# Optimization experiments

Measured on AMD Instinct MI355X. Metric: run time of the kernel, lower is better.

## Reference

```python
import jax, jax.numpy as jnp
from jax import lax
import numpy as np

N_ITERS = 200        # FISTA iterations (replaces per-row CVXPY solves)
BISECT_ITERS = 50    # bisection steps for capped-simplex projection
POWER_ITERS = 30     # power iterations for Lipschitz estimate


def _project_capped_simplex(v, lower, upper):
    """Project v (shape [N]) onto {x : sum(x)=1, lower<=x<=upper} via bisection on the dual shift tau."""
    lo = jnp.min(v) - upper
    hi = jnp.max(v) - lower

    def body(carry, _):
        lo, hi = carry
        mid = 0.5 * (lo + hi)
        s = jnp.sum(jnp.clip(v - mid, lower, upper))  # decreasing in mid
        lo = jnp.where(s > 1.0, mid, lo)
        hi = jnp.where(s > 1.0, hi, mid)
        return (lo, hi), None

    (lo, hi), _ = lax.scan(body, (lo, hi), None, length=BISECT_ITERS)
    tau = 0.5 * (lo + hi)
    return jnp.clip(v - tau, lower, upper)


def _solve_qp_batched(A, Y, lower, upper):
    """Batched solve of min_x ||x @ A - y||^2 s.t. sum(x)=1, lower<=x<=upper,
    one QP per row y of Y. A: [N,D], Y: [N,D] -> X: [N,N]. FISTA with exact
    capped-simplex projection; faithful to the per-row CVXPY QP in the source."""
    N = A.shape[0]
    Q = A @ A.T            # [N,N] Hessian/2
    C = Y @ A.T            # [N,N] linear term

    # Lipschitz constant of gradient = 2 * lambda_max(Q), via power iteration.
    v = jnp.ones((N,), A.dtype) / N

    def pw(v, _):
        w = Q @ v
        return w / (jnp.linalg.norm(w) + 1e-12), None

    v, _ = lax.scan(pw, v, None, length=POWER_ITERS)
    lmax = v @ (Q @ v)
    step = 1.0 / (2.0 * lmax + 1e-12)

    proj = jax.vmap(lambda r: _project_capped_simplex(r, lower, upper))
    X0 = jnp.full((N, N), 1.0 / N, A.dtype)  # feasible start (uniform simplex point)

    def fista(carry, _):
        X, Z, t = carry
        G = 2.0 * (Z @ Q - C)                 # grad of ||z A - y||^2 wrt z, all rows at once
        Xn = proj(Z - step * G)
        tn = 0.5 * (1.0 + jnp.sqrt(1.0 + 4.0 * t * t))
        Zn = Xn + ((t - 1.0) / tn) * (Xn - X)
        return (Xn, Zn, tn), None

    (X, _, _), _ = lax.scan(fista, (X0, X0, jnp.asarray(1.0, A.dtype)), None, length=N_ITERS)
    return X


def setup_inputs() -> dict:
    key = jax.random.key(0)
    k1, k2 = jax.random.split(key)
    N, D = 2048, 512
    fea1 = jax.random.normal(k1, (N, D), jnp.float32)
    fea2 = jax.random.normal(k2, (N, D), jnp.float32)
    return {"fea1": fea1, "fea2": fea2}


def reference(fea1, fea2):
    lower, upper = 0.0, 1.0
    nfea1 = fea1 / jnp.linalg.norm(fea1, axis=1, keepdims=True)
    nfea2 = fea2 / jnp.linalg.norm(fea2, axis=1, keepdims=True)
    # Solver operates on detached features in the original (numpy/CVXPY).
    XX = _solve_qp_batched(lax.stop_gradient(nfea2), lax.stop_gradient(nfea1), lower, upper)
    XX = lax.stop_gradient(XX)  # mirrors XX.detach() in the source
    distance = -jnp.mean((XX @ nfea2 - nfea1) ** 2)  # -MSELoss
    return distance
```

## Files before the change

kernel.cpp:

```cpp
#include <hip/hip_runtime.h>
#include <cmath>

#define N 2048
#define D 512
#define N_ITERS 200
#define NEWTON_ITERS 16
#define POWER_ITERS 30

typedef unsigned short u16;
typedef __bf16 bf16x8 __attribute__((ext_vector_type(8)));
typedef float f32x4 __attribute__((ext_vector_type(4)));

__device__ __forceinline__ float wave_reduce_sum(float x) {
#pragma unroll
  for (int o = 32; o > 0; o >>= 1) x += __shfl_xor(x, o, 64);
  return x;
}

__device__ __forceinline__ u16 f2b(float f) {
  unsigned int u = __float_as_uint(f);
  u = (u + 0x7FFFu + ((u >> 16) & 1u)) >> 16;
  return (u16)u;
}

__device__ __forceinline__ float b2f(unsigned int lo16) {
  return __uint_as_float((lo16 & 0xffffu) << 16);
}

__device__ __forceinline__ void gload16(const u16* g, u16* l) {
  __builtin_amdgcn_global_load_lds(
      (const __attribute__((address_space(1))) unsigned int*)g,
      (__attribute__((address_space(3))) unsigned int*)l, 16, 0, 0);
}

__global__ __launch_bounds__(256) void rownorm_kernel(const float* __restrict__ fea1,
                                                      const float* __restrict__ fea2,
                                                      float* __restrict__ Y,
                                                      float* __restrict__ A) {
  int b = blockIdx.x;
  int row = b & (N - 1);
  const float* src = (b < N) ? fea1 : fea2;
  float* dst = (b < N) ? Y : A;
  const float2* s2 = (const float2*)(src + (size_t)row * D);
  float2* d2 = (float2*)(dst + (size_t)row * D);
  int t = threadIdx.x;
  float2 v = s2[t];
  float ss = v.x * v.x + v.y * v.y;
  ss = wave_reduce_sum(ss);
  __shared__ float sred[4];
  int wid = t >> 6, lane = t & 63;
  if (lane == 0) sred[wid] = ss;
  __syncthreads();
  if (t == 0) sred[0] = sred[0] + sred[1] + sred[2] + sred[3];
  __syncthreads();
  float inv = 1.0f / sqrtf(sred[0]);
  d2[t] = make_float2(v.x * inv, v.y * inv);
}

__global__ __launch_bounds__(256) void prep_kernel(const float* __restrict__ A,
                                                   u16* __restrict__ Ab,
                                                   u16* __restrict__ AbT) {
  __shared__ float tile[32][33];
  int c0 = blockIdx.x * 32, r0 = blockIdx.y * 32;
  int tid = threadIdx.x;
  int r = tid >> 3, q = tid & 7;
  float4 v = *(const float4*)&A[(size_t)(r0 + r) * D + c0 + q * 4];
  tile[r][q * 4 + 0] = v.x; tile[r][q * 4 + 1] = v.y;
  tile[r][q * 4 + 2] = v.z; tile[r][q * 4 + 3] = v.w;
  ushort4 b4 = make_ushort4(f2b(v.x), f2b(v.y), f2b(v.z), f2b(v.w));
  *(ushort4*)&Ab[(size_t)(r0 + r) * D + c0 + q * 4] = b4;
  __syncthreads();
  int c = tid >> 3, qq = tid & 7;
  ushort4 t4 = make_ushort4(f2b(tile[qq * 4 + 0][c]), f2b(tile[qq * 4 + 1][c]),
                            f2b(tile[qq * 4 + 2][c]), f2b(tile[qq * 4 + 3][c]));
  *(ushort4*)&AbT[(size_t)(c0 + c) * N + r0 + qq * 4] = t4;
}

__global__ __launch_bounds__(256) void fill_init(u16* __restrict__ Zb, u16* __restrict__ Xb,
                                                 float* __restrict__ v) {
  const float c = 1.0f / (float)N;
  const unsigned int cw = (unsigned int)f2b(c);
  const unsigned int pp = cw | (cw << 16);
  size_t i = (size_t)blockIdx.x * blockDim.x + threadIdx.x;
  uint4 val = make_uint4(pp, pp, pp, pp);
  ((uint4*)Zb)[i] = val;
  ((uint4*)Xb)[i] = val;
  if (i < N) v[i] = c;
}

__global__ __launch_bounds__(256) void atv_kernel(const u16* __restrict__ Ab,
                                                  const float* __restrict__ v,
                                                  float* __restrict__ u) {
  __shared__ float part[4][64];
  int lane = threadIdx.x & 63, wid = threadIdx.x >> 6;
  int d = blockIdx.x * 64 + lane;
  float acc = 0.f;
  int r0 = wid * 512;
  for (int i = 0; i < 512; ++i) {
    int r = r0 + i;
    acc = fmaf(b2f(Ab[(size_t)r * D + d]), v[r], acc);
  }
  part[wid][lane] = acc;
  __syncthreads();
  if (wid == 0) u[d] = part[0][lane] + part[1][lane] + part[2][lane] + part[3][lane];
}

__global__ __launch_bounds__(256) void av_kernel(const u16* __restrict__ Ab,
                                                 const float* __restrict__ u,
                                                 float* __restrict__ w) {
  int wid = threadIdx.x >> 6, lane = threadIdx.x & 63;
  int row = blockIdx.x * 4 + wid;
  uint4 q = *(const uint4*)&Ab[(size_t)row * D + lane * 8];
  float4 u0 = *(const float4*)&u[lane * 8];
  float4 u1 = *(const float4*)&u[lane * 8 + 4];
  float acc = 0.f;
  acc = fmaf(b2f(q.x), u0.x, acc);
  acc = fmaf(b2f(q.x >> 16), u0.y, acc);
  acc = fmaf(b2f(q.y), u0.z, acc);
  acc = fmaf(b2f(q.y >> 16), u0.w, acc);
  acc = fmaf(b2f(q.z), u1.x, acc);
  acc = fmaf(b2f(q.z >> 16), u1.y, acc);
  acc = fmaf(b2f(q.w), u1.z, acc);
  acc = fmaf(b2f(q.w >> 16), u1.w, acc);
  acc = wave_reduce_sum(acc);
  if (lane == 0) w[row] = acc * 0.0625f;
}

__global__ __launch_bounds__(1024) void rayleigh_kernel(const float* __restrict__ v,
                                                        const float* __restrict__ w,
                                                        float* __restrict__ step) {
  int t = threadIdx.x;
  float a0 = v[t], a1 = v[t + 1024];
  float b0 = w[t], b1 = w[t + 1024];
  float s1 = a0 * b0 + a1 * b1;
  float s2 = a0 * a0 + a1 * a1;
  s1 = wave_reduce_sum(s1);
  s2 = wave_reduce_sum(s2);
  __shared__ float r1[16], r2[16];
  int wid = t >> 6, lane = t & 63;
  if (lane == 0) { r1[wid] = s1; r2[wid] = s2; }
  __syncthreads();
  if (t == 0) {
    float t1 = 0.f, t2 = 0.f;
#pragma unroll
    for (int i = 0; i < 16; ++i) { t1 += r1[i]; t2 += r2[i]; }
    float lam = 16.0f * t1 / t2;
    step[0] = 1.0f / (2.0f * lam + 1e-12f);
  }
}


template <int FOUT>
__global__ __launch_bounds__(256) void gemm1_mfma(const u16* __restrict__ Am,
                                                  const u16* __restrict__ Bm,
                                                  const float* __restrict__ Y,
                                                  u16* __restrict__ outb,
                                                  float* __restrict__ outf) {
  __shared__ u16 lds[2 * 16384];
  const int tid = threadIdx.x, lane = tid & 63, wid = tid >> 6;
  const int row0 = blockIdx.y * 64, col0 = blockIdx.x * 64;
  const int wr = (wid >> 1) * 32, wc = (wid & 1) * 32;
  const int fr = lane & 15, h = lane >> 4;
  const int grow = lane >> 4, gslot = lane & 15;
  f32x4 acc[2][2] = {};

#define G1_STAGE(BUF, T)                                                        \
  {                                                                             \
    const int k0 = (T) * 128;                                                   \
    _Pragma("unroll") for (int q = 0; q < 4; ++q) {                             \
      const int m = wid * 4 + q;                                                \
      const int r = m * 4 + grow;                                               \
      const int kl = (gslot ^ (r & 15)) * 8;                                    \
      gload16(&Am[(size_t)(row0 + r) * 2048 + k0 + kl],                         \
              &lds[(BUF) * 16384 + m * 512]);                                   \
      gload16(&Bm[(size_t)(col0 + r) * 2048 + k0 + kl],                         \
              &lds[(BUF) * 16384 + 8192 + m * 512]);                            \
    }                                                                           \
  }

  G1_STAGE(0, 0);
  __syncthreads();
#pragma unroll 2
  for (int t = 0; t < 16; ++t) {
    const int buf = (t & 1) * 16384;
    if (t < 15) G1_STAGE((t & 1) ^ 1, t + 1);
    bf16x8 af[2][4], bg[2][4];
#pragma unroll
    for (int i = 0; i < 2; ++i) {
      const int r = wr + i * 16 + fr;
#pragma unroll
      for (int ks = 0; ks < 4; ++ks)
        af[i][ks] = *(const bf16x8*)&lds[buf + r * 128 + ((((ks << 2) + h) ^ (r & 15)) << 3)];
    }
#pragma unroll
    for (int j = 0; j < 2; ++j) {
      const int c = wc + j * 16 + fr;
#pragma unroll
      for (int ks = 0; ks < 4; ++ks)
        bg[j][ks] = *(const bf16x8*)&lds[buf + 8192 + c * 128 + ((((ks << 2) + h) ^ (c & 15)) << 3)];
    }
#pragma unroll
    for (int ks = 0; ks < 4; ++ks)
#pragma unroll
      for (int i = 0; i < 2; ++i)
#pragma unroll
        for (int j = 0; j < 2; ++j)
          acc[i][j] = __builtin_amdgcn_mfma_f32_16x16x32_bf16(af[i][ks], bg[j][ks], acc[i][j], 0, 0, 0);
    __syncthreads();
  }
#pragma unroll
  for (int i = 0; i < 2; ++i)
#pragma unroll
    for (int j = 0; j < 2; ++j)
#pragma unroll
      for (int g = 0; g < 4; ++g) {
        int r = row0 + wr + i * 16 + h * 4 + g;
        int c = col0 + wc + j * 16 + fr;
        float val = acc[i][j][g] - Y[(size_t)r * D + c];
        if (FOUT) outf[(size_t)r * D + c] = val;
        else      outb[(size_t)r * D + c] = f2b(val);
      }
#undef G1_STAGE
}

__global__ __launch_bounds__(512) void gemm2_mfma(const u16* __restrict__ Tb,
                                                  const u16* __restrict__ Ab,
                                                  u16* __restrict__ Gb) {
  __shared__ u16 lds[2 * 16384];
  const int tid = threadIdx.x, lane = tid & 63, wid = tid >> 6;
  const int row0 = blockIdx.y * 128, col0 = blockIdx.x * 128;
  const int wr = (wid >> 2) * 64, wc = (wid & 3) * 32;
  const int fr = lane & 15, h = lane >> 4;
  const int grow = lane >> 3, gslot = lane & 7;
  f32x4 acc[4][2] = {};

#define G2_STAGE(BUF, T)                                                        \
  {                                                                             \
    const int k0 = (T) * 64;                                                    \
    _Pragma("unroll") for (int q = 0; q < 2; ++q) {                             \
      const int m = wid * 2 + q;                                                \
      const int r = m * 8 + grow;                                               \
      const int kl = (gslot ^ (r & 7)) * 8;                                     \
      gload16(&Tb[(size_t)(row0 + r) * 512 + k0 + kl],                          \
              &lds[(BUF) * 16384 + m * 512]);                                   \
      gload16(&Ab[(size_t)(col0 + r) * 512 + k0 + kl],                          \
              &lds[(BUF) * 16384 + 8192 + m * 512]);                            \
    }                                                                           \
  }

  G2_STAGE(0, 0);
  __syncthreads();
#pragma unroll 2
  for (int t = 0; t < 8; ++t) {
    const int buf = (t & 1) * 16384;
    if (t < 7) G2_STAGE((t & 1) ^ 1, t + 1);
    bf16x8 af[4][2], bg[2][2];
#pragma unroll
    for (int i = 0; i < 4; ++i) {
      const int r = wr + i * 16 + fr;
#pragma unroll
      for (int ks = 0; ks < 2; ++ks)
        af[i][ks] = *(const bf16x8*)&lds[buf + r * 64 + ((((ks << 2) + h) ^ (r & 7)) << 3)];
    }
#pragma unroll
    for (int j = 0; j < 2; ++j) {
      const int c = wc + j * 16 + fr;
#pragma unroll
      for (int ks = 0; ks < 2; ++ks)
        bg[j][ks] = *(const bf16x8*)&lds[buf + 8192 + c * 64 + ((((ks << 2) + h) ^ (c & 7)) << 3)];
    }
#pragma unroll
    for (int ks = 0; ks < 2; ++ks)
#pragma unroll
      for (int i = 0; i < 4; ++i)
#pragma unroll
        for (int j = 0; j < 2; ++j)
          acc[i][j] = __builtin_amdgcn_mfma_f32_16x16x32_bf16(af[i][ks], bg[j][ks], acc[i][j], 0, 0, 0);
    __syncthreads();
  }
#pragma unroll
  for (int i = 0; i < 4; ++i)
#pragma unroll
    for (int j = 0; j < 2; ++j)
#pragma unroll
      for (int g = 0; g < 4; ++g) {
        int r = row0 + wr + i * 16 + h * 4 + g;
        int c = col0 + wc + j * 16 + fr;
        Gb[(size_t)r * N + c] = f2b(acc[i][j][g]);
      }
#undef G2_STAGE
}

__global__ __launch_bounds__(256) void prox_kernel(const u16* __restrict__ Gb,
                                                   u16* __restrict__ Zb,
                                                   u16* __restrict__ Xb,
                                                   const float* __restrict__ stepp,
                                                   float beta) {
  const int wid = threadIdx.x >> 6, lane = threadIdx.x & 63;
  const int row = blockIdx.x * 4 + wid;
  const size_t rb = (size_t)row * N;
  const float s2 = 2.0f * stepp[0];
  float v[32], xo[32];
  float mn = 1e30f, mx = -1e30f;
#pragma unroll
  for (int c = 0; c < 4; ++c) {
    const int base = c * 512 + lane * 8;
    uint4 zu = *(const uint4*)&Zb[rb + base];
    uint4 gu = *(const uint4*)&Gb[rb + base];
    uint4 xu = *(const uint4*)&Xb[rb + base];
    const unsigned int zw[4] = {zu.x, zu.y, zu.z, zu.w};
    const unsigned int gw[4] = {gu.x, gu.y, gu.z, gu.w};
    const unsigned int xw[4] = {xu.x, xu.y, xu.z, xu.w};
#pragma unroll
    for (int w = 0; w < 4; ++w) {
      int e = c * 8 + w * 2;
      float v0 = b2f(zw[w]) - s2 * b2f(gw[w]);
      float v1 = __uint_as_float(zw[w] & 0xffff0000u) - s2 * __uint_as_float(gw[w] & 0xffff0000u);
      v[e] = v0; v[e + 1] = v1;
      xo[e] = b2f(xw[w]); xo[e + 1] = __uint_as_float(xw[w] & 0xffff0000u);
      mn = fminf(mn, fminf(v0, v1));
      mx = fmaxf(mx, fmaxf(v0, v1));
    }
  }
#pragma unroll
  for (int o = 32; o > 0; o >>= 1) {
    mn = fminf(mn, __shfl_xor(mn, o, 64));
    mx = fmaxf(mx, __shfl_xor(mx, o, 64));
  }
  float lo = mn - 1.0f, hi = mx;
  float mid = 0.5f * (lo + hi);
#pragma unroll 1
  for (int it = 0; it < NEWTON_ITERS; ++it) {
    float s = 0.f, cnt = 0.f;
#pragma unroll
    for (int e = 0; e < 32; ++e) {
      float d = v[e] - mid;
      s += fminf(fmaxf(d, 0.f), 1.f);
      cnt += (d > 0.f && d < 1.f) ? 1.f : 0.f;
    }
    s = wave_reduce_sum(s);
    cnt = wave_reduce_sum(cnt);
    bool gt = s > 1.0f;
    lo = gt ? mid : lo;
    hi = gt ? hi : mid;
    float prop = mid + (s - 1.0f) / fmaxf(cnt, 0.5f);
    mid = (prop > lo && prop < hi) ? prop : 0.5f * (lo + hi);
  }
  float tau = mid;
#pragma unroll
  for (int c = 0; c < 4; ++c) {
    const int base = c * 512 + lane * 8;
    unsigned int xp[4], zp[4];
#pragma unroll
    for (int q = 0; q < 8; ++q) {
      int e = c * 8 + q;
      float x = fminf(fmaxf(v[e] - tau, 0.f), 1.f);
      float zn = x + beta * (x - xo[e]);
      unsigned int xb = (unsigned int)f2b(x);
      unsigned int zb = (unsigned int)f2b(zn);
      if (q & 1) { xp[q >> 1] |= xb << 16; zp[q >> 1] |= zb << 16; }
      else       { xp[q >> 1] = xb;        zp[q >> 1] = zb; }
    }
    *(uint4*)&Xb[rb + base] = make_uint4(xp[0], xp[1], xp[2], xp[3]);
    *(uint4*)&Zb[rb + base] = make_uint4(zp[0], zp[1], zp[2], zp[3]);
  }
}

__global__ void zero_out_kernel(float* __restrict__ out) {
  if (threadIdx.x == 0 && blockIdx.x == 0) out[0] = 0.f;
}

__global__ __launch_bounds__(256) void mse_reduce_kernel(const float* __restrict__ T,
                                                         float* __restrict__ out) {
  size_t i = (size_t)blockIdx.x * blockDim.x + threadIdx.x;
  size_t total = (size_t)N * D;
  size_t stride = (size_t)gridDim.x * blockDim.x;
  float acc = 0.f;
  for (size_t idx = i; idx < total; idx += stride) {
    float t = T[idx];
    acc = fmaf(t, t, acc);
  }
  acc = wave_reduce_sum(acc);
  __shared__ float sred[4];
  int wid = threadIdx.x >> 6, lane = threadIdx.x & 63;
  if (lane == 0) sred[wid] = acc;
  __syncthreads();
  if (threadIdx.x == 0) {
    float tot = sred[0] + sred[1] + sred[2] + sred[3];
    atomicAdd(out, -tot / (float)((size_t)N * D));
  }
}

extern "C" void kernel_launch(void* const* d_in, const int* in_sizes, int n_in,
                              void* d_out, int out_size, void* d_ws, size_t ws_size,
                              hipStream_t stream) {
  const float* fea1 = (const float*)d_in[0];
  const float* fea2 = (const float*)d_in[1];
  float* out = (float*)d_out;
  float* ws = (float*)d_ws;

  float* A   = ws;
  float* Y   = A + (size_t)N * D;
  float* T32 = Y + (size_t)N * D;
  float* vv  = T32 + (size_t)N * D;
  float* wv  = vv + N;
  float* uu  = wv + N;
  float* sp  = uu + D;
  u16* Zb    = (u16*)(sp + 16);
  u16* Gb    = Zb + (size_t)N * N;
  u16* Xb    = Gb + (size_t)N * N;
  u16* Tb    = Xb + (size_t)N * N;
  u16* Ab    = Tb + (size_t)N * D;
  u16* AbT   = Ab + (size_t)N * D;

  rownorm_kernel<<<2 * N, 256, 0, stream>>>(fea1, fea2, Y, A);
  prep_kernel<<<dim3(D / 32, N / 32), 256, 0, stream>>>(A, Ab, AbT);
  fill_init<<<(N * N / 8) / 256, 256, 0, stream>>>(Zb, Xb, vv);

  float* pv = vv;
  float* pw = wv;
  for (int it = 0; it < POWER_ITERS; ++it) {
    atv_kernel<<<D / 64, 256, 0, stream>>>(Ab, pv, uu);
    av_kernel<<<N / 4, 256, 0, stream>>>(Ab, uu, pw);
    float* tmp = pv; pv = pw; pw = tmp;
  }
  atv_kernel<<<D / 64, 256, 0, stream>>>(Ab, pv, uu);
  av_kernel<<<N / 4, 256, 0, stream>>>(Ab, uu, pw);
  rayleigh_kernel<<<1, 1024, 0, stream>>>(pv, pw, sp);

  float t = 1.0f;
  for (int it = 0; it < N_ITERS; ++it) {
    float tn = 0.5f * (1.0f + sqrtf(1.0f + 4.0f * t * t));
    float beta = (t - 1.0f) / tn;
    t = tn;
    gemm1_mfma<0><<<dim3(D / 64, N / 64), 256, 0, stream>>>(Zb, AbT, Y, Tb, T32);
    gemm2_mfma<<<dim3(N / 128, N / 128), 512, 0, stream>>>(Tb, Ab, Gb);
    prox_kernel<<<N / 4, 256, 0, stream>>>(Gb, Zb, Xb, sp, beta);
  }

  gemm1_mfma<1><<<dim3(D / 64, N / 64), 256, 0, stream>>>(Xb, AbT, Y, Tb, T32);
  zero_out_kernel<<<1, 64, 0, stream>>>(out);
  mse_reduce_kernel<<<512, 256, 0, stream>>>(T32, out);
}
```

Baseline: 10.44 ms.

## Fuse FISTA loop into one persistent kernel with grid barriers

```diff
diff --git a/kernel.cpp b/kernel.cpp
--- a/kernel.cpp
+++ b/kernel.cpp
@@ -6,6 +6,7 @@
 #define N_ITERS 200
 #define NEWTON_ITERS 16
 #define POWER_ITERS 30
+#define NBLOCKS 256
 
 typedef unsigned short u16;
 typedef __bf16 bf16x8 __attribute__((ext_vector_type(8)));
@@ -31,6 +32,23 @@
   __builtin_amdgcn_global_load_lds(
       (const __attribute__((address_space(1))) unsigned int*)g,
       (__attribute__((address_space(3))) unsigned int*)l, 16, 0, 0);
+}
+
+__device__ __forceinline__ void grid_barrier(unsigned int* bar) {
+  __syncthreads();
+  if (threadIdx.x == 0) {
+    unsigned int g = __hip_atomic_load(&bar[1], __ATOMIC_RELAXED, __HIP_MEMORY_SCOPE_AGENT);
+    unsigned int a = __hip_atomic_fetch_add(&bar[0], 1u, __ATOMIC_ACQ_REL, __HIP_MEMORY_SCOPE_AGENT);
+    if (a + 1u == (unsigned int)NBLOCKS) {
+      __hip_atomic_store(&bar[0], 0u, __ATOMIC_RELAXED, __HIP_MEMORY_SCOPE_AGENT);
+      __hip_atomic_store(&bar[1], g + 1u, __ATOMIC_RELEASE, __HIP_MEMORY_SCOPE_AGENT);
+    } else {
+      while (__hip_atomic_load(&bar[1], __ATOMIC_ACQUIRE, __HIP_MEMORY_SCOPE_AGENT) == g) {
+        __builtin_amdgcn_s_sleep(8);
+      }
+    }
+  }
+  __syncthreads();
 }
 
 __global__ __launch_bounds__(256) void rownorm_kernel(const float* __restrict__ fea1,
@@ -77,7 +95,8 @@
 }
 
 __global__ __launch_bounds__(256) void fill_init(u16* __restrict__ Zb, u16* __restrict__ Xb,
-                                                 float* __restrict__ v) {
+                                                 float* __restrict__ v,
+                                                 unsigned int* __restrict__ bar) {
   const float c = 1.0f / (float)N;
   const unsigned int cw = (unsigned int)f2b(c);
   const unsigned int pp = cw | (cw << 16);
@@ -86,6 +105,7 @@
   ((uint4*)Zb)[i] = val;
   ((uint4*)Xb)[i] = val;
   if (i < N) v[i] = c;
+  if (i < 4) bar[i] = 0u;
 }
 
 __global__ __launch_bounds__(256) void atv_kernel(const u16* __restrict__ Ab,
@@ -151,40 +171,37 @@
 
 
 template <int FOUT>
-__global__ __launch_bounds__(256) void gemm1_mfma(const u16* __restrict__ Am,
-                                                  const u16* __restrict__ Bm,
-                                                  const float* __restrict__ Y,
-                                                  u16* __restrict__ outb,
-                                                  float* __restrict__ outf) {
-  __shared__ u16 lds[2 * 16384];
-  const int tid = threadIdx.x, lane = tid & 63, wid = tid >> 6;
-  const int row0 = blockIdx.y * 64, col0 = blockIdx.x * 64;
-  const int wr = (wid >> 1) * 32, wc = (wid & 1) * 32;
+__device__ __forceinline__ void phase_g1(u16* lds, const u16* __restrict__ Am,
+                                         const u16* __restrict__ Bm,
+                                         const float* __restrict__ Y,
+                                         u16* __restrict__ outb, float* __restrict__ outf,
+                                         int bid, int tid) {
+  const int lane = tid & 63, wid = tid >> 6;
+  const int row0 = (bid >> 3) * 64, col0 = (bid & 7) * 64;
+  const int wr = (wid >> 2) * 32, wc = (wid & 3) * 16;
   const int fr = lane & 15, h = lane >> 4;
   const int grow = lane >> 4, gslot = lane & 15;
-  f32x4 acc[2][2] = {};
-
-#define G1_STAGE(BUF, T)                                                        \
-  {                                                                             \
-    const int k0 = (T) * 128;                                                   \
-    _Pragma("unroll") for (int q = 0; q < 4; ++q) {                             \
-      const int m = wid * 4 + q;                                                \
-      const int r = m * 4 + grow;                                               \
-      const int kl = (gslot ^ (r & 15)) * 8;                                    \
-      gload16(&Am[(size_t)(row0 + r) * 2048 + k0 + kl],                         \
-              &lds[(BUF) * 16384 + m * 512]);                                   \
-      gload16(&Bm[(size_t)(col0 + r) * 2048 + k0 + kl],                         \
-              &lds[(BUF) * 16384 + 8192 + m * 512]);                            \
-    }                                                                           \
-  }
-
-  G1_STAGE(0, 0);
+  f32x4 acc[2] = {};
+
+#define G1S(BUF, T)                                                              \
+  {                                                                              \
+    const int k0 = (T) * 128;                                                    \
+    _Pragma("unroll") for (int q = 0; q < 2; ++q) {                              \
+      const int m = wid * 2 + q;                                                 \
+      const int r = m * 4 + grow;                                                \
+      const int kl = (gslot ^ (r & 15)) * 8;                                     \
+      gload16(&Am[(size_t)(row0 + r) * 2048 + k0 + kl], &lds[(BUF)*16384 + m*512]);        \
+      gload16(&Bm[(size_t)(col0 + r) * 2048 + k0 + kl], &lds[(BUF)*16384 + 8192 + m*512]); \
+    }                                                                            \
+  }
+
+  G1S(0, 0);
   __syncthreads();
 #pragma unroll 2
   for (int t = 0; t < 16; ++t) {
     const int buf = (t & 1) * 16384;
-    if (t < 15) G1_STAGE((t & 1) ^ 1, t + 1);
-    bf16x8 af[2][4], bg[2][4];
+    if (t < 15) G1S((t & 1) ^ 1, t + 1);
+    bf16x8 af[2][4], bg[4];
 #pragma unroll
     for (int i = 0; i < 2; ++i) {
       const int r = wr + i * 16 + fr;
@@ -192,68 +209,60 @@
       for (int ks = 0; ks < 4; ++ks)
         af[i][ks] = *(const bf16x8*)&lds[buf + r * 128 + ((((ks << 2) + h) ^ (r & 15)) << 3)];
     }
-#pragma unroll
-    for (int j = 0; j < 2; ++j) {
-      const int c = wc + j * 16 + fr;
+    {
+      const int c = wc + fr;
 #pragma unroll
       for (int ks = 0; ks < 4; ++ks)
-        bg[j][ks] = *(const bf16x8*)&lds[buf + 8192 + c * 128 + ((((ks << 2) + h) ^ (c & 15)) << 3)];
+        bg[ks] = *(const bf16x8*)&lds[buf + 8192 + c * 128 + ((((ks << 2) + h) ^ (c & 15)) << 3)];
     }
 #pragma unroll
     for (int ks = 0; ks < 4; ++ks)
 #pragma unroll
       for (int i = 0; i < 2; ++i)
-#pragma unroll
-        for (int j = 0; j < 2; ++j)
-          acc[i][j] = __builtin_amdgcn_mfma_f32_16x16x32_bf16(af[i][ks], bg[j][ks], acc[i][j], 0, 0, 0);
+        acc[i] = __builtin_amdgcn_mfma_f32_16x16x32_bf16(af[i][ks], bg[ks], acc[i], 0, 0, 0);
     __syncthreads();
   }
 #pragma unroll
   for (int i = 0; i < 2; ++i)
 #pragma unroll
-    for (int j = 0; j < 2; ++j)
-#pragma unroll
-      for (int g = 0; g < 4; ++g) {
-        int r = row0 + wr + i * 16 + h * 4 + g;
-        int c = col0 + wc + j * 16 + fr;
-        float val = acc[i][j][g] - Y[(size_t)r * D + c];
-        if (FOUT) outf[(size_t)r * D + c] = val;
-        else      outb[(size_t)r * D + c] = f2b(val);
-      }
-#undef G1_STAGE
-}
-
-__global__ __launch_bounds__(512) void gemm2_mfma(const u16* __restrict__ Tb,
-                                                  const u16* __restrict__ Ab,
-                                                  u16* __restrict__ Gb) {
-  __shared__ u16 lds[2 * 16384];
-  const int tid = threadIdx.x, lane = tid & 63, wid = tid >> 6;
-  const int row0 = blockIdx.y * 128, col0 = blockIdx.x * 128;
+    for (int g = 0; g < 4; ++g) {
+      int r = row0 + wr + i * 16 + h * 4 + g;
+      int c = col0 + wc + fr;
+      float val = acc[i][g] - Y[(size_t)r * D + c];
+      if (FOUT) outf[(size_t)r * D + c] = val;
+      else      outb[(size_t)r * D + c] = f2b(val);
+    }
+#undef G1S
+}
+
+__device__ __forceinline__ void phase_g2(u16* lds, const u16* __restrict__ Tb,
+                                         const u16* __restrict__ Ab,
+                                         u16* __restrict__ Gb, int bid, int tid) {
+  const int lane = tid & 63, wid = tid >> 6;
+  const int row0 = (bid >> 4) * 128, col0 = (bid & 15) * 128;
   const int wr = (wid >> 2) * 64, wc = (wid & 3) * 32;
   const int fr = lane & 15, h = lane >> 4;
   const int grow = lane >> 3, gslot = lane & 7;
   f32x4 acc[4][2] = {};
 
-#define G2_STAGE(BUF, T)                                                        \
-  {                                                                             \
-    const int k0 = (T) * 64;                                                    \
-    _Pragma("unroll") for (int q = 0; q < 2; ++q) {                             \
-      const int m = wid * 2 + q;                                                \
-      const int r = m * 8 + grow;                                               \
-      const int kl = (gslot ^ (r & 7)) * 8;                                     \
-      gload16(&Tb[(size_t)(row0 + r) * 512 + k0 + kl],                          \
-              &lds[(BUF) * 16384 + m * 512]);                                   \
-      gload16(&Ab[(size_t)(col0 + r) * 512 + k0 + kl],                          \
-              &lds[(BUF) * 16384 + 8192 + m * 512]);                            \
-    }                                                                           \
-  }
-
-  G2_STAGE(0, 0);
+#define G2S(BUF, T)                                                              \
+  {                                                                              \
+    const int k0 = (T) * 64;                                                     \
+    _Pragma("unroll") for (int q = 0; q < 2; ++q) {                              \
+      const int m = wid * 2 + q;                                                 \
+      const int r = m * 8 + grow;                                                \
+      const int kl = (gslot ^ (r & 7)) * 8;                                      \
+      gload16(&Tb[(size_t)(row0 + r) * 512 + k0 + kl], &lds[(BUF)*16384 + m*512]);         \
+      gload16(&Ab[(size_t)(col0 + r) * 512 + k0 + kl], &lds[(BUF)*16384 + 8192 + m*512]);  \
+    }                                                                            \
+  }
+
+  G2S(0, 0);
   __syncthreads();
 #pragma unroll 2
   for (int t = 0; t < 8; ++t) {
     const int buf = (t & 1) * 16384;
-    if (t < 7) G2_STAGE((t & 1) ^ 1, t + 1);
+    if (t < 7) G2S((t & 1) ^ 1, t + 1);
     bf16x8 af[4][2], bg[2][2];
 #pragma unroll
     for (int i = 0; i < 4; ++i) {
@@ -288,18 +297,15 @@
         int c = col0 + wc + j * 16 + fr;
         Gb[(size_t)r * N + c] = f2b(acc[i][j][g]);
       }
-#undef G2_STAGE
-}
-
-__global__ __launch_bounds__(256) void prox_kernel(const u16* __restrict__ Gb,
-                                                   u16* __restrict__ Zb,
-                                                   u16* __restrict__ Xb,
-                                                   const float* __restrict__ stepp,
-                                                   float beta) {
-  const int wid = threadIdx.x >> 6, lane = threadIdx.x & 63;
-  const int row = blockIdx.x * 4 + wid;
+#undef G2S
+}
+
+__device__ __forceinline__ void phase_prox(const u16* __restrict__ Gb,
+                                           u16* __restrict__ Zb, u16* __restrict__ Xb,
+                                           float s2, float beta, int bid, int tid) {
+  const int wid = tid >> 6, lane = tid & 63;
+  const int row = bid * 8 + wid;
   const size_t rb = (size_t)row * N;
-  const float s2 = 2.0f * stepp[0];
   float v[32], xo[32];
   float mn = 1e30f, mx = -1e30f;
 #pragma unroll
@@ -364,6 +370,34 @@
     *(uint4*)&Xb[rb + base] = make_uint4(xp[0], xp[1], xp[2], xp[3]);
     *(uint4*)&Zb[rb + base] = make_uint4(zp[0], zp[1], zp[2], zp[3]);
   }
+}
+
+__global__ __launch_bounds__(512) void fista_kernel(const u16* __restrict__ Ab,
+                                                    const u16* __restrict__ AbT,
+                                                    const float* __restrict__ Y,
+                                                    u16* __restrict__ Zb,
+                                                    u16* __restrict__ Gb,
+                                                    u16* __restrict__ Xb,
+                                                    u16* __restrict__ Tb,
+                                                    float* __restrict__ T32,
+                                                    const float* __restrict__ sp,
+                                                    unsigned int* __restrict__ bar) {
+  __shared__ u16 lds[2 * 16384];
+  const int bid = blockIdx.x, tid = threadIdx.x;
+  const float s2 = 2.0f * sp[0];
+  float t = 1.0f;
+  for (int it = 0; it < N_ITERS; ++it) {
+    float tn = 0.5f * (1.0f + sqrtf(1.0f + 4.0f * t * t));
+    float beta = (t - 1.0f) / tn;
+    t = tn;
+    phase_g1<0>(lds, Zb, AbT, Y, Tb, T32, bid, tid);
+    grid_barrier(bar);
+    phase_g2(lds, Tb, Ab, Gb, bid, tid);
+    grid_barrier(bar);
+    phase_prox(Gb, Zb, Xb, s2, beta, bid, tid);
+    grid_barrier(bar);
+  }
+  phase_g1<1>(lds, Xb, AbT, Y, Tb, T32, bid, tid);
 }
 
 __global__ void zero_out_kernel(float* __restrict__ out) {
@@ -406,7 +440,8 @@
   float* wv  = vv + N;
   float* uu  = wv + N;
   float* sp  = uu + D;
-  u16* Zb    = (u16*)(sp + 16);
+  unsigned int* bar = (unsigned int*)(sp + 8);
+  u16* Zb    = (u16*)(bar + 8);
   u16* Gb    = Zb + (size_t)N * N;
   u16* Xb    = Gb + (size_t)N * N;
   u16* Tb    = Xb + (size_t)N * N;
@@ -415,7 +450,7 @@
 
   rownorm_kernel<<<2 * N, 256, 0, stream>>>(fea1, fea2, Y, A);
   prep_kernel<<<dim3(D / 32, N / 32), 256, 0, stream>>>(A, Ab, AbT);
-  fill_init<<<(N * N / 8) / 256, 256, 0, stream>>>(Zb, Xb, vv);
+  fill_init<<<(N * N / 8) / 256, 256, 0, stream>>>(Zb, Xb, vv, bar);
 
   float* pv = vv;
   float* pw = wv;
@@ -428,17 +463,8 @@
   av_kernel<<<N / 4, 256, 0, stream>>>(Ab, uu, pw);
   rayleigh_kernel<<<1, 1024, 0, stream>>>(pv, pw, sp);
 
-  float t = 1.0f;
-  for (int it = 0; it < N_ITERS; ++it) {
-    float tn = 0.5f * (1.0f + sqrtf(1.0f + 4.0f * t * t));
-    float beta = (t - 1.0f) / tn;
-    t = tn;
-    gemm1_mfma<0><<<dim3(D / 64, N / 64), 256, 0, stream>>>(Zb, AbT, Y, Tb, T32);
-    gemm2_mfma<<<dim3(N / 128, N / 128), 512, 0, stream>>>(Tb, Ab, Gb);
-    prox_kernel<<<N / 4, 256, 0, stream>>>(Gb, Zb, Xb, sp, beta);
-  }
-
-  gemm1_mfma<1><<<dim3(D / 64, N / 64), 256, 0, stream>>>(Xb, AbT, Y, Tb, T32);
+  fista_kernel<<<NBLOCKS, 512, 0, stream>>>(Ab, AbT, Y, Zb, Gb, Xb, Tb, T32, sp, bar);
+
   zero_out_kernel<<<1, 64, 0, stream>>>(out);
   mse_reduce_kernel<<<512, 256, 0, stream>>>(T32, out);
 }
```

Result: slower. 30.70 ms (+194.0%).
